# Optimization experiments

Measured on AMD Instinct MI355X. Metric: run time of the kernel, lower is better.

## Reference

```python
import jax, jax.numpy as jnp
import numpy as np

N_NODES = 100000
N_EDGES = 1600000
D = 64
ED = 16
N_LAYERS = 3
NEG_SLOPE = 0.2


def gat_conv(x, src, dst, ea, W, a_src, a_dst, W_e, a_e, b):
    """Single-head PyG GATConv with edge_dim, self-loops already appended."""
    N = x.shape[0]
    h = x @ W                                   # [N, D]
    s_src = h @ a_src                           # [N]
    s_dst = h @ a_dst                           # [N]
    s_edge = (ea @ W_e) @ a_e                   # [Etot]
    alpha = s_src[src] + s_dst[dst] + s_edge    # [Etot]
    alpha = jnp.where(alpha >= 0, alpha, NEG_SLOPE * alpha)  # leaky_relu(0.2)
    # segment softmax over destination node
    m = jax.ops.segment_max(alpha, dst, num_segments=N)
    e = jnp.exp(alpha - m[dst])
    z = jax.ops.segment_sum(e, dst, num_segments=N)
    w = e / z[dst]                              # [Etot]
    out = jax.ops.segment_sum(w[:, None] * h[src], dst, num_segments=N)
    return out + b


def setup_inputs() -> dict:
    key = jax.random.key(0)
    ks = jax.random.split(key, 8)
    sc = 1.0 / np.sqrt(D)
    return {
        "x": jax.random.normal(ks[0], (N_NODES, D), jnp.float32),
        "edge_index": jax.random.randint(ks[1], (2, N_EDGES), 0, N_NODES, jnp.int32),
        "edge_attr": jax.random.normal(ks[2], (N_EDGES, ED), jnp.float32),
        "Ws": jax.random.normal(ks[3], (N_LAYERS, D, D), jnp.float32) * sc,
        "att_srcs": jax.random.normal(ks[4], (N_LAYERS, D), jnp.float32) * sc,
        "att_dsts": jax.random.normal(ks[5], (N_LAYERS, D), jnp.float32) * sc,
        "W_edges": jax.random.normal(ks[6], (N_LAYERS, ED, D), jnp.float32) * sc,
        "att_edges": jax.random.normal(ks[7], (N_LAYERS, D), jnp.float32) * sc,
        "biases": jnp.zeros((N_LAYERS, D), jnp.float32),
        "batch_size": 100,
    }


def reference(x, edge_index, edge_attr, Ws, att_srcs, att_dsts, W_edges, att_edges, biases, batch_size):
    N = x.shape[0]
    # add self loops (PyG fill_value='mean' for self-loop edge_attr)
    loops = jnp.arange(N, dtype=edge_index.dtype)
    src = jnp.concatenate([edge_index[0], loops])
    dst = jnp.concatenate([edge_index[1], loops])
    ea = jnp.concatenate(
        [edge_attr, jnp.broadcast_to(edge_attr.mean(0), (N, edge_attr.shape[1]))], axis=0
    )
    for l in range(N_LAYERS):
        x = gat_conv(x, src, dst, ea, Ws[l], att_srcs[l], att_dsts[l],
                     W_edges[l], att_edges[l], biases[l])
        x = jax.nn.gelu(x, approximate=False)  # torch F.gelu default = exact
        # dropout is identity in eval mode
    return x.reshape(batch_size, N // batch_size, D)
```

## Files before the change

kernel.cpp:

```cpp
#include <hip/hip_runtime.h>
#include <math.h>

#define NN 100000
#define NE 1600000
#define ET (NN + NE)
#define D 64
#define EDIM 16

static __device__ __forceinline__ float leaky(float a) { return a >= 0.f ? a : 0.2f * a; }

static __device__ __forceinline__ unsigned fmap(float f) {
    unsigned u = __float_as_uint(f);
    return (u & 0x80000000u) ? ~u : (u | 0x80000000u);
}
static __device__ __forceinline__ float funmap(unsigned u) {
    unsigned f = (u & 0x80000000u) ? (u ^ 0x80000000u) : ~u;
    return __uint_as_float(f);
}

__global__ __launch_bounds__(256) void k_init(int* __restrict__ deg, float* __restrict__ meansum,
                                              unsigned* __restrict__ gse_u, unsigned* __restrict__ gsrc_u,
                                              float* __restrict__ w16, const float* __restrict__ We,
                                              const float* __restrict__ ae) {
    int i = blockIdx.x * 256 + threadIdx.x;
    if (i < NN) deg[i] = 1;
    if (blockIdx.x == 0) {
        int t = threadIdx.x;
        if (t < 16) meansum[t] = 0.f;
        if (t < 3) {
            gse_u[t] = fmap(-3.0e38f);
            gsrc_u[t] = fmap(-3.0e38f);
        }
        if (t < 48) {
            int l = t >> 4, k = t & 15;
            const float* wr = We + l * (EDIM * D) + k * D;
            const float* av = ae + l * D;
            float s = 0.f;
#pragma unroll
            for (int j = 0; j < D; j++) s += wr[j] * av[j];
            w16[t] = s;
        }
    }
}

__global__ __launch_bounds__(256) void k_edge(const int* __restrict__ ei, const float* __restrict__ ea,
                                              const float* __restrict__ w16, int* __restrict__ deg,
                                              unsigned short* __restrict__ rank16,
                                              float* __restrict__ sedge3, float* __restrict__ meansum,
                                              unsigned* __restrict__ gse_u) {
    int tid = blockIdx.x * blockDim.x + threadIdx.x;
    int stride = gridDim.x * blockDim.x;
    float wr[48];
#pragma unroll
    for (int c = 0; c < 48; c++) wr[c] = w16[c];
    float ms[16];
#pragma unroll
    for (int c = 0; c < 16; c++) ms[c] = 0.f;
    float smax[3] = {-3e38f, -3e38f, -3e38f};
    for (int e = tid; e < NE; e += stride) {
        int d = ei[NE + e];
        int rank = atomicAdd(&deg[d], 1);
        rank16[e] = (unsigned short)rank;
        const float4* ea4 = (const float4*)(ea + (size_t)e * EDIM);
        float4 v0 = ea4[0], v1 = ea4[1], v2 = ea4[2], v3 = ea4[3];
        float vv[16] = {v0.x, v0.y, v0.z, v0.w, v1.x, v1.y, v1.z, v1.w,
                        v2.x, v2.y, v2.z, v2.w, v3.x, v3.y, v3.z, v3.w};
#pragma unroll
        for (int c = 0; c < 16; c++) ms[c] += vv[c];
#pragma unroll
        for (int l = 0; l < 3; l++) {
            float s = 0.f;
#pragma unroll
            for (int c = 0; c < 16; c++) s += vv[c] * wr[l * 16 + c];
            sedge3[(size_t)l * NE + e] = s;
            smax[l] = fmaxf(smax[l], s);
        }
    }
#pragma unroll
    for (int c = 0; c < 16; c++)
        for (int o = 32; o; o >>= 1) ms[c] += __shfl_xor(ms[c], o);
#pragma unroll
    for (int l = 0; l < 3; l++)
        for (int o = 32; o; o >>= 1) smax[l] = fmaxf(smax[l], __shfl_xor(smax[l], o));
    __shared__ float bsum[16];
    __shared__ unsigned bmax[3];
    if (threadIdx.x < 16) bsum[threadIdx.x] = 0.f;
    if (threadIdx.x < 3) bmax[threadIdx.x] = fmap(-3e38f);
    __syncthreads();
    if ((threadIdx.x & 63) == 0) {
        for (int c = 0; c < 16; c++) atomicAdd(&bsum[c], ms[c]);
        for (int l = 0; l < 3; l++) atomicMax(&bmax[l], fmap(smax[l]));
    }
    __syncthreads();
    if (threadIdx.x < 16) atomicAdd(&meansum[threadIdx.x], bsum[threadIdx.x]);
    if (threadIdx.x < 3) atomicMax(&gse_u[threadIdx.x], bmax[threadIdx.x]);
}

__global__ __launch_bounds__(256) void k_scan1(const int* __restrict__ deg, int* __restrict__ rowstart,
                                               int* __restrict__ blocksum) {
    __shared__ int sd[256];
    int t = threadIdx.x;
    int i = blockIdx.x * 256 + t;
    int v = (i < NN) ? deg[i] : 0;
    sd[t] = v;
    __syncthreads();
    for (int o = 1; o < 256; o <<= 1) {
        int x = sd[t];
        int y = (t >= o) ? sd[t - o] : 0;
        __syncthreads();
        sd[t] = x + y;
        __syncthreads();
    }
    int incl = sd[t];
    if (i < NN) rowstart[i] = incl - v;
    if (t == 255) blocksum[blockIdx.x] = incl;
}

__global__ __launch_bounds__(512) void k_scan2(const int* __restrict__ blocksum, int* __restrict__ blockoff,
                                               int* __restrict__ rowstart, const float* __restrict__ meansum,
                                               const float* __restrict__ w16, float* __restrict__ slw,
                                               const unsigned* __restrict__ gse_u, float* __restrict__ gse_f,
                                               int nb) {
    __shared__ int sd[512];
    int t = threadIdx.x;
    int v = (t < nb) ? blocksum[t] : 0;
    sd[t] = v;
    __syncthreads();
    for (int o = 1; o < 512; o <<= 1) {
        int x = sd[t];
        int y = (t >= o) ? sd[t - o] : 0;
        __syncthreads();
        sd[t] = x + y;
        __syncthreads();
    }
    if (t < nb) blockoff[t] = sd[t] - v;
    if (t == 0) rowstart[NN] = ET;
    if (t < 3) {
        float s = 0.f;
        for (int k = 0; k < 16; k++) s += (meansum[k] * (1.0f / NE)) * w16[t * 16 + k];
        slw[t] = s;
        gse_f[t] = fmaxf(funmap(gse_u[t]), s);
    }
}

__global__ __launch_bounds__(256) void k_scan3(int* __restrict__ rowstart, const int* __restrict__ blockoff) {
    int i = blockIdx.x * 256 + threadIdx.x;
    if (i < NN) rowstart[i] = rowstart[i] + blockoff[i >> 8];
}

__global__ __launch_bounds__(256) void k_scatter(const int* __restrict__ ei, const float* __restrict__ sedge3,
                                                 const float* __restrict__ slw,
                                                 const unsigned short* __restrict__ rank16,
                                                 const int* __restrict__ rowstart, float4* __restrict__ csr) {
    int tid = blockIdx.x * blockDim.x + threadIdx.x;
    int stride = gridDim.x * blockDim.x;
    float s0 = slw[0], s1 = slw[1], s2 = slw[2];
    for (int e = tid; e < ET; e += stride) {
        int s, d, pos;
        float a0, a1, a2;
        if (e < NE) {
            s = ei[e];
            d = ei[NE + e];
            a0 = sedge3[e];
            a1 = sedge3[(size_t)NE + e];
            a2 = sedge3[2 * (size_t)NE + e];
            pos = rowstart[d] + rank16[e];
        } else {
            s = d = e - NE;
            a0 = s0; a1 = s1; a2 = s2;
            pos = rowstart[d];
        }
        csr[pos] = make_float4(__int_as_float(s), a0, a1, a2);
    }
}

__global__ __launch_bounds__(256) void k_gemm(const float* __restrict__ x, const float* __restrict__ W,
                                              const float* __restrict__ asrc, const float* __restrict__ adst,
                                              float* __restrict__ h, float* __restrict__ ssrc,
                                              float* __restrict__ sdst, unsigned* __restrict__ gsrcu) {
    int t = threadIdx.x;
    int lane = t & 63;
    int wv = __builtin_amdgcn_readfirstlane(t >> 6);
    int row0 = blockIdx.x * 64 + wv * 16;
    float Wreg[64];
#pragma unroll
    for (int k = 0; k < 64; k++) Wreg[k] = W[k * 64 + lane];
    float asl = asrc[lane], adl = adst[lane];
    float wmax = -3e38f;
    for (int rr = 0; rr < 16; rr++) {
        int r = row0 + rr;
        if (r >= NN) break;
        const float* xr = x + (size_t)r * 64;
        float acc = 0.f;
#pragma unroll
        for (int k = 0; k < 64; k++) acc = fmaf(xr[k], Wreg[k], acc);
        h[(size_t)r * 64 + lane] = acc;
        float ps = acc * asl, pd = acc * adl;
#pragma unroll
        for (int o = 32; o; o >>= 1) {
            ps += __shfl_xor(ps, o);
            pd += __shfl_xor(pd, o);
        }
        wmax = fmaxf(wmax, ps);
        if (lane == 0) {
            ssrc[r] = ps;
            sdst[r] = pd;
        }
    }
    if (lane == 0) atomicMax(gsrcu, fmap(wmax));
}

template <int LAYER>
__global__ __launch_bounds__(256) void k_agg(const float4* __restrict__ csr, const int* __restrict__ rowstart,
                                             const float* __restrict__ ssrc, const float* __restrict__ sdst,
                                             const float* __restrict__ h, const float* __restrict__ bias,
                                             const unsigned* __restrict__ gsrcu, const float* __restrict__ gsef,
                                             float* __restrict__ out) {
    int t = threadIdx.x;
    int lane = t & 63;
    int wv = __builtin_amdgcn_readfirstlane(t >> 6);
    int n = blockIdx.x * 4 + wv;
    int start = rowstart[n];
    int dg = rowstart[n + 1] - start;
    float sd = sdst[n];
    float M = leaky(funmap(gsrcu[0]) + sd + gsef[LAYER]);
    float acc = 0.f, z = 0.f;
    for (int base = 0; base < dg; base += 64) {
        int i = base + lane;
        float ew = 0.f;
        int es = 0;
        if (i < dg) {
            float4 rec = csr[start + i];
            float se = (LAYER == 0) ? rec.y : ((LAYER == 1) ? rec.z : rec.w);
            es = __float_as_int(rec.x);
            ew = __expf(leaky(ssrc[es] + sd + se) - M);
        }
        z += ew;
        int cnt = min(64, dg - base);
        if (cnt == 64) {
#pragma unroll 4
            for (int j = 0; j < 64; j++) {
                float wj = __shfl(ew, j);
                int sj = __shfl(es, j);
                acc = fmaf(wj, h[(size_t)sj * 64 + lane], acc);
            }
        } else {
            for (int j = 0; j < cnt; j++) {
                float wj = __shfl(ew, j);
                int sj = __shfl(es, j);
                acc = fmaf(wj, h[(size_t)sj * 64 + lane], acc);
            }
        }
    }
#pragma unroll
    for (int o = 32; o; o >>= 1) z += __shfl_xor(z, o);
    float v = acc / z + bias[lane];
    float g = 0.5f * v * (1.0f + erff(v * 0.70710678118654752f));
    out[(size_t)n * 64 + lane] = g;
}

extern "C" void kernel_launch(void* const* d_in, const int* in_sizes, int n_in,
                              void* d_out, int out_size, void* d_ws, size_t ws_size,
                              hipStream_t stream) {
    const float* x0 = (const float*)d_in[0];
    const int* ei = (const int*)d_in[1];
    const float* ea = (const float*)d_in[2];
    const float* Ws = (const float*)d_in[3];
    const float* asrc = (const float*)d_in[4];
    const float* adst = (const float*)d_in[5];
    const float* We = (const float*)d_in[6];
    const float* ae = (const float*)d_in[7];
    const float* bias = (const float*)d_in[8];

    char* wsb = (char*)d_ws;
    size_t off = 0;
    auto alloc = [&](size_t bytes) -> char* {
        char* p = wsb + off;
        off += (bytes + 255) & ~(size_t)255;
        return p;
    };
    float* xA = (float*)alloc((size_t)NN * D * 4);
    float* xB = (float*)alloc((size_t)NN * D * 4);
    float* h = (float*)alloc((size_t)NN * D * 4);
    float* ssrc = (float*)alloc((size_t)NN * 4);
    float* sdst = (float*)alloc((size_t)NN * 4);
    float* sedge3 = (float*)alloc(3 * (size_t)NE * 4);
    float4* csr = (float4*)alloc((size_t)ET * 16);
    unsigned short* rank16 = (unsigned short*)alloc((size_t)NE * 2);
    int* deg = (int*)alloc((size_t)NN * 4);
    int* rowstart = (int*)alloc((size_t)(NN + 1) * 4);
    int* blocksum = (int*)alloc(512 * 4);
    int* blockoff = (int*)alloc(512 * 4);
    float* meansum = (float*)alloc(16 * 4);
    float* w16 = (float*)alloc(48 * 4);
    float* slw = (float*)alloc(3 * 4);
    unsigned* gse_u = (unsigned*)alloc(3 * 4);
    float* gse_f = (float*)alloc(3 * 4);
    unsigned* gsrc_u = (unsigned*)alloc(3 * 4);

    int nb = (NN + 255) / 256;
    k_init<<<nb, 256, 0, stream>>>(deg, meansum, gse_u, gsrc_u, w16, We, ae);
    k_edge<<<1024, 256, 0, stream>>>(ei, ea, w16, deg, rank16, sedge3, meansum, gse_u);
    k_scan1<<<nb, 256, 0, stream>>>(deg, rowstart, blocksum);
    k_scan2<<<1, 512, 0, stream>>>(blocksum, blockoff, rowstart, meansum, w16, slw, gse_u, gse_f, nb);
    k_scan3<<<nb, 256, 0, stream>>>(rowstart, blockoff);
    k_scatter<<<2048, 256, 0, stream>>>(ei, sedge3, slw, rank16, rowstart, csr);

    float* outp = (float*)d_out;
    int gg = (NN + 63) / 64;
    k_gemm<<<gg, 256, 0, stream>>>(x0, Ws, asrc, adst, h, ssrc, sdst, gsrc_u + 0);
    k_agg<0><<<NN / 4, 256, 0, stream>>>(csr, rowstart, ssrc, sdst, h, bias, gsrc_u + 0, gse_f, xA);
    k_gemm<<<gg, 256, 0, stream>>>(xA, Ws + 4096, asrc + 64, adst + 64, h, ssrc, sdst, gsrc_u + 1);
    k_agg<1><<<NN / 4, 256, 0, stream>>>(csr, rowstart, ssrc, sdst, h, bias + 64, gsrc_u + 1, gse_f, xB);
    k_gemm<<<gg, 256, 0, stream>>>(xB, Ws + 8192, asrc + 128, adst + 128, h, ssrc, sdst, gsrc_u + 2);
    k_agg<2><<<NN / 4, 256, 0, stream>>>(csr, rowstart, ssrc, sdst, h, bias + 128, gsrc_u + 2, gse_f, outp);
}
```

Baseline: 910.4 us.

## Bucket CSR scatter in two phases and vectorize aggregation gathers as float4

k_edge now writes the source id and the three edge scores as one packed float4 record, plus a packed (dst, rank) word, instead of separate arrays. The CSR scatter is split into two phases. The first appends records into buckets of 128 destination nodes, staged in the unused xA/xB buffers. The second writes each bucket into its final CSR positions, so global writes land in a more local region. The aggregation kernel now has each lane load a float4 slice of h and processes 4 edges per wavefront step, then combines the partial sums with cross-lane shuffles. This raises memory-level parallelism on the gathers, at the cost of an extra reduction, a tail that reads zero-weight padding rows, and an extra staging pass with atomics.

```diff
diff --git a/kernel.cpp b/kernel.cpp
--- a/kernel.cpp
+++ b/kernel.cpp
@@ -6,6 +6,8 @@
 #define ET (NN + NE)
 #define D 64
 #define EDIM 16
+#define BSH 7
+#define NB ((NN + 127) >> BSH)
 
 static __device__ __forceinline__ float leaky(float a) { return a >= 0.f ? a : 0.2f * a; }
 
@@ -18,12 +20,14 @@
     return __uint_as_float(f);
 }
 
-__global__ __launch_bounds__(256) void k_init(int* __restrict__ deg, float* __restrict__ meansum,
+__global__ __launch_bounds__(256) void k_init(int* __restrict__ deg, int* __restrict__ bcur,
+                                              float* __restrict__ meansum,
                                               unsigned* __restrict__ gse_u, unsigned* __restrict__ gsrc_u,
                                               float* __restrict__ w16, const float* __restrict__ We,
                                               const float* __restrict__ ae) {
     int i = blockIdx.x * 256 + threadIdx.x;
     if (i < NN) deg[i] = 1;
+    if (i < NB) bcur[i] = 0;
     if (blockIdx.x == 0) {
         int t = threadIdx.x;
         if (t < 16) meansum[t] = 0.f;
@@ -45,8 +49,8 @@
 
 __global__ __launch_bounds__(256) void k_edge(const int* __restrict__ ei, const float* __restrict__ ea,
                                               const float* __restrict__ w16, int* __restrict__ deg,
-                                              unsigned short* __restrict__ rank16,
-                                              float* __restrict__ sedge3, float* __restrict__ meansum,
+                                              unsigned* __restrict__ pack,
+                                              float4* __restrict__ rec4, float* __restrict__ meansum,
                                               unsigned* __restrict__ gse_u) {
     int tid = blockIdx.x * blockDim.x + threadIdx.x;
     int stride = gridDim.x * blockDim.x;
@@ -58,23 +62,26 @@
     for (int c = 0; c < 16; c++) ms[c] = 0.f;
     float smax[3] = {-3e38f, -3e38f, -3e38f};
     for (int e = tid; e < NE; e += stride) {
+        int s = ei[e];
         int d = ei[NE + e];
-        int rank = atomicAdd(&deg[d], 1);
-        rank16[e] = (unsigned short)rank;
+        unsigned rank = (unsigned)atomicAdd(&deg[d], 1);
+        pack[e] = ((unsigned)d << 15) | rank;
         const float4* ea4 = (const float4*)(ea + (size_t)e * EDIM);
         float4 v0 = ea4[0], v1 = ea4[1], v2 = ea4[2], v3 = ea4[3];
         float vv[16] = {v0.x, v0.y, v0.z, v0.w, v1.x, v1.y, v1.z, v1.w,
                         v2.x, v2.y, v2.z, v2.w, v3.x, v3.y, v3.z, v3.w};
 #pragma unroll
         for (int c = 0; c < 16; c++) ms[c] += vv[c];
+        float sl[3];
 #pragma unroll
         for (int l = 0; l < 3; l++) {
-            float s = 0.f;
-#pragma unroll
-            for (int c = 0; c < 16; c++) s += vv[c] * wr[l * 16 + c];
-            sedge3[(size_t)l * NE + e] = s;
-            smax[l] = fmaxf(smax[l], s);
-        }
+            float sv = 0.f;
+#pragma unroll
+            for (int c = 0; c < 16; c++) sv = fmaf(vv[c], wr[l * 16 + c], sv);
+            sl[l] = sv;
+            smax[l] = fmaxf(smax[l], sv);
+        }
+        rec4[e] = make_float4(__int_as_float(s), sl[0], sl[1], sl[2]);
     }
 #pragma unroll
     for (int c = 0; c < 16; c++)
@@ -148,29 +155,45 @@
     if (i < NN) rowstart[i] = rowstart[i] + blockoff[i >> 8];
 }
 
-__global__ __launch_bounds__(256) void k_scatter(const int* __restrict__ ei, const float* __restrict__ sedge3,
-                                                 const float* __restrict__ slw,
-                                                 const unsigned short* __restrict__ rank16,
-                                                 const int* __restrict__ rowstart, float4* __restrict__ csr) {
+__global__ __launch_bounds__(256) void k_scatA(const float4* __restrict__ rec4,
+                                               const unsigned* __restrict__ pack,
+                                               const float* __restrict__ slw,
+                                               const int* __restrict__ rowstart,
+                                               int* __restrict__ bcur,
+                                               float4* __restrict__ st4, int* __restrict__ stpos) {
     int tid = blockIdx.x * blockDim.x + threadIdx.x;
     int stride = gridDim.x * blockDim.x;
     float s0 = slw[0], s1 = slw[1], s2 = slw[2];
     for (int e = tid; e < ET; e += stride) {
-        int s, d, pos;
-        float a0, a1, a2;
+        float4 rec;
+        int d, rank;
         if (e < NE) {
-            s = ei[e];
-            d = ei[NE + e];
-            a0 = sedge3[e];
-            a1 = sedge3[(size_t)NE + e];
-            a2 = sedge3[2 * (size_t)NE + e];
-            pos = rowstart[d] + rank16[e];
+            rec = rec4[e];
+            unsigned p = pack[e];
+            d = (int)(p >> 15);
+            rank = (int)(p & 32767u);
         } else {
-            s = d = e - NE;
-            a0 = s0; a1 = s1; a2 = s2;
-            pos = rowstart[d];
-        }
-        csr[pos] = make_float4(__int_as_float(s), a0, a1, a2);
+            d = e - NE;
+            rank = 0;
+            rec = make_float4(__int_as_float(d), s0, s1, s2);
+        }
+        int pos = rowstart[d] + rank;
+        int bb = rowstart[d & ~127];
+        int c = atomicAdd(&bcur[d >> BSH], 1);
+        st4[bb + c] = rec;
+        stpos[bb + c] = pos;
+    }
+}
+
+__global__ __launch_bounds__(256) void k_scatB(const float4* __restrict__ st4,
+                                               const int* __restrict__ stpos,
+                                               const int* __restrict__ rowstart,
+                                               float4* __restrict__ csr) {
+    int b = blockIdx.x;
+    int lo = rowstart[b << BSH];
+    int hi = (b == NB - 1) ? ET : rowstart[(b + 1) << BSH];
+    for (int i = lo + threadIdx.x; i < hi; i += 256) {
+        csr[stpos[i]] = st4[i];
     }
 }
 
@@ -224,7 +247,10 @@
     int dg = rowstart[n + 1] - start;
     float sd = sdst[n];
     float M = leaky(funmap(gsrcu[0]) + sd + gsef[LAYER]);
-    float acc = 0.f, z = 0.f;
+    int g = lane >> 4;
+    int fslice = (lane & 15) * 4;
+    float4 acc = make_float4(0.f, 0.f, 0.f, 0.f);
+    float z = 0.f;
     for (int base = 0; base < dg; base += 64) {
         int i = base + lane;
         float ew = 0.f;
@@ -237,26 +263,42 @@
         }
         z += ew;
         int cnt = min(64, dg - base);
-        if (cnt == 64) {
 #pragma unroll 4
-            for (int j = 0; j < 64; j++) {
-                float wj = __shfl(ew, j);
-                int sj = __shfl(es, j);
-                acc = fmaf(wj, h[(size_t)sj * 64 + lane], acc);
-            }
-        } else {
-            for (int j = 0; j < cnt; j++) {
-                float wj = __shfl(ew, j);
-                int sj = __shfl(es, j);
-                acc = fmaf(wj, h[(size_t)sj * 64 + lane], acc);
-            }
-        }
+        for (int js = 0; js < cnt; js += 4) {
+            int j = js + g;
+            float wj = __shfl(ew, j);
+            int sj = __shfl(es, j);
+            float4 hv = *(const float4*)(h + (size_t)sj * 64 + fslice);
+            acc.x = fmaf(wj, hv.x, acc.x);
+            acc.y = fmaf(wj, hv.y, acc.y);
+            acc.z = fmaf(wj, hv.z, acc.z);
+            acc.w = fmaf(wj, hv.w, acc.w);
+        }
+    }
+#pragma unroll
+    for (int o = 16; o <= 32; o <<= 1) {
+        acc.x += __shfl_xor(acc.x, o);
+        acc.y += __shfl_xor(acc.y, o);
+        acc.z += __shfl_xor(acc.z, o);
+        acc.w += __shfl_xor(acc.w, o);
     }
 #pragma unroll
     for (int o = 32; o; o >>= 1) z += __shfl_xor(z, o);
-    float v = acc / z + bias[lane];
-    float g = 0.5f * v * (1.0f + erff(v * 0.70710678118654752f));
-    out[(size_t)n * 64 + lane] = g;
+    if (lane < 16) {
+        float inv = 1.f / z;
+        float4 bv = *(const float4*)(bias + fslice);
+        float4 v;
+        v.x = acc.x * inv + bv.x;
+        v.y = acc.y * inv + bv.y;
+        v.z = acc.z * inv + bv.z;
+        v.w = acc.w * inv + bv.w;
+        const float k = 0.70710678118654752f;
+        v.x = 0.5f * v.x * (1.0f + erff(v.x * k));
+        v.y = 0.5f * v.y * (1.0f + erff(v.y * k));
+        v.z = 0.5f * v.z * (1.0f + erff(v.z * k));
+        v.w = 0.5f * v.w * (1.0f + erff(v.w * k));
+        *(float4*)(out + (size_t)n * 64 + fslice) = v;
+    }
 }
 
 extern "C" void kernel_launch(void* const* d_in, const int* in_sizes, int n_in,
@@ -284,9 +326,9 @@
     float* h = (float*)alloc((size_t)NN * D * 4);
     float* ssrc = (float*)alloc((size_t)NN * 4);
     float* sdst = (float*)alloc((size_t)NN * 4);
-    float* sedge3 = (float*)alloc(3 * (size_t)NE * 4);
+    float4* rec4 = (float4*)alloc((size_t)NE * 16);
     float4* csr = (float4*)alloc((size_t)ET * 16);
-    unsigned short* rank16 = (unsigned short*)alloc((size_t)NE * 2);
+    unsigned* pack = (unsigned*)alloc((size_t)NE * 4);
     int* deg = (int*)alloc((size_t)NN * 4);
     int* rowstart = (int*)alloc((size_t)(NN + 1) * 4);
     int* blocksum = (int*)alloc(512 * 4);
@@ -297,14 +339,18 @@
     unsigned* gse_u = (unsigned*)alloc(3 * 4);
     float* gse_f = (float*)alloc(3 * 4);
     unsigned* gsrc_u = (unsigned*)alloc(3 * 4);
+    int* bcur = (int*)alloc((size_t)NB * 4);
+    float4* st4 = (float4*)xA;
+    int* stpos = (int*)(xA + 4 * (size_t)ET);
 
     int nb = (NN + 255) / 256;
-    k_init<<<nb, 256, 0, stream>>>(deg, meansum, gse_u, gsrc_u, w16, We, ae);
-    k_edge<<<1024, 256, 0, stream>>>(ei, ea, w16, deg, rank16, sedge3, meansum, gse_u);
+    k_init<<<nb, 256, 0, stream>>>(deg, bcur, meansum, gse_u, gsrc_u, w16, We, ae);
+    k_edge<<<1024, 256, 0, stream>>>(ei, ea, w16, deg, pack, rec4, meansum, gse_u);
     k_scan1<<<nb, 256, 0, stream>>>(deg, rowstart, blocksum);
     k_scan2<<<1, 512, 0, stream>>>(blocksum, blockoff, rowstart, meansum, w16, slw, gse_u, gse_f, nb);
     k_scan3<<<nb, 256, 0, stream>>>(rowstart, blockoff);
-    k_scatter<<<2048, 256, 0, stream>>>(ei, sedge3, slw, rank16, rowstart, csr);
+    k_scatA<<<2048, 256, 0, stream>>>(rec4, pack, slw, rowstart, bcur, st4, stpos);
+    k_scatB<<<NB, 256, 0, stream>>>(st4, stpos, rowstart, csr);
 
     float* outp = (float*)d_out;
     int gg = (NN + 63) / 64;
```

Result: slower. 1.199 ms (+31.7%).
